# Optimization experiments

Measured on AMD Instinct MI355X. Metric: run time of the kernel, lower is better.

## Reference

```python
import jax, jax.numpy as jnp
import numpy as np

B, N, D, H, L, M, V, F = 4, 2048, 1024, 16, 4, 256, 32000, 4096
DH = D // H  # 64
KEPS = 1e-4  # performer softmax-kernel eps


def layer_norm(x, g, b, eps=1e-5):
    mu = x.mean(-1, keepdims=True)
    var = ((x - mu) ** 2).mean(-1, keepdims=True)
    return (x - mu) * jax.lax.rsqrt(var + eps) * g + b


def softmax_kernel(data, proj, is_query):
    # data: [B,H,N,DH], proj: [M,DH] -> phi(data): [B,H,N,M]
    dn = data.shape[-1] ** -0.25  # d^{-1/4} normalizer
    ratio = proj.shape[0] ** -0.5
    dd = jnp.einsum('bhnd,md->bhnm', dn * data, proj)
    diag = (data * data).sum(-1, keepdims=True) * 0.5 * dn * dn
    if is_query:
        mx = jnp.max(dd, axis=-1, keepdims=True)
    else:
        mx = jnp.max(dd, axis=(-2, -1), keepdims=True)
    return ratio * (jnp.exp(dd - diag - mx) + KEPS)


def setup_inputs() -> dict:
    key = jax.random.key(0)
    ks = iter(jax.random.split(key, 16))
    p = lambda shape: jax.random.normal(next(ks), shape, jnp.float32) * 0.02
    return {
        'x': jax.random.randint(next(ks), (B, N), 0, V, jnp.int32),
        'mask': jnp.ones((B, N), jnp.bool_),
        'tok_emb': p((V, D)),
        'pos_emb': p((N, D)),
        'ln1_g': jnp.ones((L, D), jnp.float32), 'ln1_b': jnp.zeros((L, D), jnp.float32),
        'wq': p((L, D, D)), 'bq': jnp.zeros((L, D), jnp.float32),
        'wk': p((L, D, D)), 'bk': jnp.zeros((L, D), jnp.float32),
        'wv': p((L, D, D)), 'bv': jnp.zeros((L, D), jnp.float32),
        'wo': p((L, D, D)), 'bo': jnp.zeros((L, D), jnp.float32),
        'proj': jax.random.normal(next(ks), (L, M, DH), jnp.float32),
        'ln2_g': jnp.ones((L, D), jnp.float32), 'ln2_b': jnp.zeros((L, D), jnp.float32),
        'w1': p((L, D, F)), 'b1': jnp.zeros((L, F), jnp.float32),
        'w2': p((L, F, D)), 'b2': jnp.zeros((L, D), jnp.float32),
    }


def reference(x, mask, tok_emb, pos_emb, ln1_g, ln1_b, wq, bq, wk, bk, wv, bv,
              wo, bo, proj, ln2_g, ln2_b, w1, b1, w2, b2):
    h = tok_emb[x] + pos_emb[jnp.arange(N)]  # [B,N,D]
    mask4 = mask[:, None, :, None]  # [B,1,N,1]

    def split_heads(t):  # [B,N,D] -> [B,H,N,DH]
        return t.reshape(B, N, H, DH).transpose(0, 2, 1, 3)

    def layer(h, params):
        (g1, c1, Wq, Bq, Wk, Bk, Wv, Bv, Wo, Bo, P, g2, c2, W1, B1, W2, B2) = params
        z = layer_norm(h, g1, c1)
        q = split_heads(z @ Wq + Bq)
        k = split_heads(z @ Wk + Bk)
        v = split_heads(z @ Wv + Bv)
        v = jnp.where(mask4, v, 0.0)  # performer masks only v
        qp = softmax_kernel(q, P, True)   # [B,H,N,M]
        kp = softmax_kernel(k, P, False)  # [B,H,N,M]
        d_inv = 1.0 / jnp.einsum('bhnm,bhm->bhn', qp, kp.sum(-2))
        ctx = jnp.einsum('bhnm,bhnd->bhmd', kp, v)  # [B,H,M,DH]
        attn = jnp.einsum('bhmd,bhnm,bhn->bhnd', ctx, qp, d_inv)
        attn = attn.transpose(0, 2, 1, 3).reshape(B, N, D)
        h = h + attn @ Wo + Bo
        z = layer_norm(h, g2, c2)
        h = h + jax.nn.gelu(z @ W1 + B1, approximate=False) @ W2 + B2
        return h, None

    h, _ = jax.lax.scan(layer, h, (ln1_g, ln1_b, wq, bq, wk, bk, wv, bv,
                                   wo, bo, proj, ln2_g, ln2_b, w1, b1, w2, b2))
    return h.mean(1)  # [B,D]
```

## Files before the change

### kernel.cpp

```cpp
#include <hip/hip_runtime.h>
#include <hip/hip_bf16.h>

typedef unsigned short u16;
typedef unsigned int u32;
typedef __attribute__((ext_vector_type(8))) short short8v;
typedef __attribute__((ext_vector_type(4))) float f32x4;

#define BB    4
#define NN    2048
#define DDIM  1024
#define HH    16
#define DH    64
#define MM    256
#define FDIM  4096
#define LL    4
#define QLD   3072

static constexpr float DN_    = 0.35355339059327373f;
static constexpr float RATIO_ = 0.0625f;
static constexpr float KEPS_  = 1e-4f;

__device__ __forceinline__ short f2bs(float f) {
  __hip_bfloat16 h = __float2bfloat16(f);
  return *(short*)&h;
}
__device__ __forceinline__ float bs2f(short s) {
  return __uint_as_float(((unsigned)(u16)s) << 16);
}
__device__ __forceinline__ float erf_fast(float x) {
  float ax = fabsf(x);
  float t = 1.f / (1.f + 0.3275911f * ax);
  float y = t * (0.254829592f + t * (-0.284496736f + t * (1.421413741f +
            t * (-1.453152027f + t * 1.061405429f))));
  float r = 1.f - y * __expf(-ax * ax);
  return copysignf(r, x);
}

__device__ __forceinline__ void gload_lds16(const void* g, void* l) {
  __builtin_amdgcn_global_load_lds(
      (const __attribute__((address_space(1))) u32*)g,
      (__attribute__((address_space(3))) u32*)l, 16, 0, 0);
}

__global__ __launch_bounds__(256) void k_sentinel(float* __restrict__ out, float val) {
  int i = blockIdx.x * 256 + threadIdx.x;
  if (i < BB * DDIM) out[i] = val;
}

__global__ __launch_bounds__(256) void k_embed_ln(const int* __restrict__ x,
    const float* __restrict__ tok, const float* __restrict__ pos,
    const float* __restrict__ g, const float* __restrict__ b,
    float* __restrict__ h, __hip_bfloat16* __restrict__ zb) {
  int r = blockIdx.x, t = threadIdx.x;
  int n = r & (NN - 1);
  int id = x[r];
  const float* tr = tok + (size_t)id * DDIM;
  const float* pr = pos + (size_t)n * DDIM;
  float* hr = h + (size_t)r * DDIM;
  float v[4], s = 0.f, s2 = 0.f;
#pragma unroll
  for (int i = 0; i < 4; i++) {
    int d = t + i * 256;
    v[i] = tr[d] + pr[d];
    hr[d] = v[i];
    s += v[i]; s2 += v[i] * v[i];
  }
#pragma unroll
  for (int o = 32; o > 0; o >>= 1) { s += __shfl_down(s, o); s2 += __shfl_down(s2, o); }
  __shared__ float ws[8];
  int wid = t >> 6, lane = t & 63;
  if (lane == 0) { ws[wid] = s; ws[4 + wid] = s2; }
  __syncthreads();
  s = ws[0] + ws[1] + ws[2] + ws[3];
  s2 = ws[4] + ws[5] + ws[6] + ws[7];
  float mu = s * (1.f / DDIM);
  float var = s2 * (1.f / DDIM) - mu * mu;
  float rstd = rsqrtf(var + 1e-5f);
  __hip_bfloat16* orow = zb + (size_t)r * DDIM;
#pragma unroll
  for (int i = 0; i < 4; i++) {
    int d = t + i * 256;
    orow[d] = __float2bfloat16((v[i] - mu) * rstd * g[d] + b[d]);
  }
}

__global__ __launch_bounds__(256) void k_ln(const float* __restrict__ in,
    const float* __restrict__ g, const float* __restrict__ b,
    __hip_bfloat16* __restrict__ out) {
  int r = blockIdx.x, t = threadIdx.x;
  const float* xr = in + (size_t)r * DDIM;
  float v[4], s = 0.f, s2 = 0.f;
#pragma unroll
  for (int i = 0; i < 4; i++) {
    v[i] = xr[t + i * 256];
    s += v[i]; s2 += v[i] * v[i];
  }
#pragma unroll
  for (int o = 32; o > 0; o >>= 1) { s += __shfl_down(s, o); s2 += __shfl_down(s2, o); }
  __shared__ float ws[8];
  int wid = t >> 6, lane = t & 63;
  if (lane == 0) { ws[wid] = s; ws[4 + wid] = s2; }
  __syncthreads();
  s = ws[0] + ws[1] + ws[2] + ws[3];
  s2 = ws[4] + ws[5] + ws[6] + ws[7];
  float mu = s * (1.f / DDIM);
  float var = s2 * (1.f / DDIM) - mu * mu;
  float rstd = rsqrtf(var + 1e-5f);
  __hip_bfloat16* orow = out + (size_t)r * DDIM;
#pragma unroll
  for (int i = 0; i < 4; i++) {
    int d = t + i * 256;
    orow[d] = __float2bfloat16((v[i] - mu) * rstd * g[d] + b[d]);
  }
}

__global__ __launch_bounds__(256) void k_wtall(const float* __restrict__ Wq,
    const float* __restrict__ Wk, const float* __restrict__ Wv,
    const float* __restrict__ Wo, const float* __restrict__ W1,
    const float* __restrict__ W2, const float* __restrict__ bq,
    const float* __restrict__ bk, const float* __restrict__ bv,
    __hip_bfloat16* __restrict__ wt, float* __restrict__ bcat) {
  int id = blockIdx.x;
  int t = threadIdx.x;
  if (id >= 3072) {
    int i = (id - 3072) * 256 + t;
    bcat[i] = i < 1024 ? bq[i] : (i < 2048 ? bk[i - 1024] : bv[i - 2048]);
    return;
  }
  const float* W;
  __hip_bfloat16* Wt;
  int K, N, n0, k0;
  if (id < 1024) {
    int which = id >> 8, local = id & 255;
    W = which == 0 ? Wq : which == 1 ? Wk : which == 2 ? Wv : Wo;
    Wt = wt + (size_t)which * 1048576;
    K = 1024; N = 1024;
    n0 = (local & 15) * 64; k0 = (local >> 4) * 64;
  } else if (id < 2048) {
    int local = id - 1024;
    W = W1; Wt = wt + (size_t)4 * 1048576;
    K = 1024; N = 4096;
    n0 = (local & 63) * 64; k0 = (local >> 6) * 64;
  } else {
    int local = id - 2048;
    W = W2; Wt = wt + (size_t)8 * 1048576;
    K = 4096; N = 1024;
    n0 = (local & 15) * 64; k0 = (local >> 4) * 64;
  }
  __shared__ float tl[64][68];
#pragma unroll
  for (int i = 0; i < 4; i++) {
    int kl = (t >> 4) + i * 16;
    float4 f = *(const float4*)&W[(size_t)(k0 + kl) * N + n0 + (t & 15) * 4];
    tl[kl][(t & 15) * 4 + 0] = f.x;
    tl[kl][(t & 15) * 4 + 1] = f.y;
    tl[kl][(t & 15) * 4 + 2] = f.z;
    tl[kl][(t & 15) * 4 + 3] = f.w;
  }
  __syncthreads();
  int nl = t >> 2;
#pragma unroll
  for (int i = 0; i < 4; i++) {
    int kl = (t & 3) * 4 + i * 16;
    size_t ob = (size_t)(n0 + nl) * K + k0 + kl;
    Wt[ob + 0] = __float2bfloat16(tl[kl + 0][nl]);
    Wt[ob + 1] = __float2bfloat16(tl[kl + 1][nl]);
    Wt[ob + 2] = __float2bfloat16(tl[kl + 2][nl]);
    Wt[ob + 3] = __float2bfloat16(tl[kl + 3][nl]);
  }
}

template <bool GELU, bool RES, bool OUTF32>
__global__ __launch_bounds__(256) void k_gemm_mfma(
    const u16* __restrict__ A, const u16* __restrict__ Bt,
    const float* __restrict__ bias, const float* __restrict__ Cin,
    void* __restrict__ Cout, int M, int K, int Nc) {
  __shared__ short As[2][128 * 32];
  __shared__ short Bs[2][128 * 32];
  int t = threadIdx.x;
  int lane = t & 63, w = t >> 6;
  int wr = w >> 1, wc = w & 1;
  int nwg = gridDim.x * gridDim.y;
  int id = blockIdx.y * gridDim.x + blockIdx.x;
  int swz = (id & 7) * (nwg >> 3) + (id >> 3);
  int bx = swz % gridDim.x, by = swz / gridDim.x;
  int row0 = by * 128, col0 = bx * 128;
  f32x4 acc[4][4];
  f32x4 z4 = {0.f, 0.f, 0.f, 0.f};
#pragma unroll
  for (int i = 0; i < 4; i++)
#pragma unroll
    for (int j = 0; j < 4; j++) acc[i][j] = z4;
  int fr = lane & 15;
  int fc = lane >> 4;
  int offA[4], offB[4];
#pragma unroll
  for (int f = 0; f < 4; f++) {
    int ra = wr * 64 + f * 16 + fr;
    offA[f] = ra * 32 + (fc ^ ((ra >> 1) & 3)) * 8;
    int rb = wc * 64 + f * 16 + fr;
    offB[f] = rb * 32 + (fc ^ ((rb >> 1) & 3)) * 8;
  }
  int c0 = t, c1 = 256 + t;
  int r0 = c0 >> 2, cl0 = (c0 & 3) ^ ((r0 >> 1) & 3);
  int r1 = c1 >> 2, cl1 = (c1 & 3) ^ ((r1 >> 1) & 3);
  const u16* pA0 = A + (size_t)(row0 + r0) * K + cl0 * 8;
  const u16* pA1 = A + (size_t)(row0 + r1) * K + cl1 * 8;
  const u16* pB0 = Bt + (size_t)(col0 + r0) * K + cl0 * 8;
  const u16* pB1 = Bt + (size_t)(col0 + r1) * K + cl1 * 8;

  auto STG = [&](short* Ab, short* Bb) {
    gload_lds16(pA0, Ab + c0 * 8);
    gload_lds16(pA1, Ab + c1 * 8);
    gload_lds16(pB0, Bb + c0 * 8);
    gload_lds16(pB1, Bb + c1 * 8);
    pA0 += 32; pA1 += 32; pB0 += 32; pB1 += 32;
  };
  auto COMPUTE = [&](const short* Ab, const short* Bb) {
    short8v af[4], bfr[4];
#pragma unroll
    for (int f = 0; f < 4; f++) {
      af[f] = *(const short8v*)(Ab + offA[f]);
      bfr[f] = *(const short8v*)(Bb + offB[f]);
    }
#pragma unroll
    for (int fi = 0; fi < 4; fi++)
#pragma unroll
      for (int fj = 0; fj < 4; fj++)
        acc[fi][fj] = __builtin_amdgcn_mfma_f32_16x16x32_bf16(
            af[fi], bfr[fj], acc[fi][fj], 0, 0, 0);
  };

  int KT = K >> 5;
  STG(As[0], Bs[0]);
  __syncthreads();
  for (int kt = 0; kt < KT - 2; kt += 2) {
    STG(As[1], Bs[1]);
    COMPUTE(As[0], Bs[0]);
    __syncthreads();
    STG(As[0], Bs[0]);
    COMPUTE(As[1], Bs[1]);
    __syncthreads();
  }
  STG(As[1], Bs[1]);
  COMPUTE(As[0], Bs[0]);
  __syncthreads();
  COMPUTE(As[1], Bs[1]);
#pragma unroll
  for (int fi = 0; fi < 4; fi++) {
#pragma unroll
    for (int fj = 0; fj < 4; fj++) {
#pragma unroll
      for (int ri = 0; ri < 4; ri++) {
        int row = row0 + wr * 64 + fi * 16 + (lane >> 4) * 4 + ri;
        int col = col0 + wc * 64 + fj * 16 + fr;
        float vv = acc[fi][fj][ri] + bias[col];
        if (GELU) vv = 0.5f * vv * (1.f + erf_fast(vv * 0.70710678118f));
        if (RES) vv += Cin[(size_t)row * Nc + col];
        if (OUTF32) ((float*)Cout)[(size_t)row * Nc + col] = vv;
        else ((__hip_bfloat16*)Cout)[(size_t)row * Nc + col] = __float2bfloat16(vv);
      }
    }
  }
}

__global__ __launch_bounds__(256) void k_kv(const u16* __restrict__ kq,
    const u16* __restrict__ vq, const float* __restrict__ P,
    float* __restrict__ es, float* __restrict__ mxc, float* __restrict__ svc,
    float* __restrict__ ctx_part) {
  int bh = blockIdx.x >> 3;
  int chunk = (blockIdx.x >> 1) & 3;
  int mh = blockIdx.x & 1;
  int b = bh >> 4, hh = bh & 15;
  int t = threadIdx.x, lane = t & 63, w = t >> 6;
  int fr = lane & 15, kc = lane >> 4;
  __shared__ short Pl[128 * 64];
  __shared__ short ksl[32 * 64];
  __shared__ short vtl[64 * 32];
  __shared__ short kpl[128 * 32];
  __shared__ float dgs[32];
  __shared__ float wredk[4];
  __shared__ float svl[32][64];
#pragma unroll
  for (int i = 0; i < 4; i++) {
    int e = i * 256 + t;
    int m = e >> 3, j = e & 7;
    const float* src = P + (size_t)(mh * 128 + m) * 64 + j * 8;
    float4 f0 = *(const float4*)src;
    float4 f1 = *(const float4*)(src + 4);
    short* dst = Pl + m * 64 + ((j ^ (m & 7)) << 3);
    dst[0] = f2bs(f0.x); dst[1] = f2bs(f0.y); dst[2] = f2bs(f0.z); dst[3] = f2bs(f0.w);
    dst[4] = f2bs(f1.x); dst[5] = f2bs(f1.y); dst[6] = f2bs(f1.z); dst[7] = f2bs(f1.w);
  }
  f32x4 z4 = {0.f, 0.f, 0.f, 0.f};
  f32x4 accc[2][4];
#pragma unroll
  for (int i = 0; i < 2; i++)
#pragma unroll
    for (int j = 0; j < 4; j++) accc[i][j] = z4;
  float ksp[2] = {0.f, 0.f};
  float svp[8] = {0.f, 0.f, 0.f, 0.f, 0.f, 0.f, 0.f, 0.f};
  float m_run = -3e38f;
  int r8 = t >> 3, j8 = t & 7;
  for (int tile = 0; tile < 16; ++tile) {
    int n0 = chunk * 512 + tile * 32;
    __syncthreads();
    {
      size_t gk = ((size_t)(b * NN) + n0 + r8) * QLD + hh * 64 + j8 * 8;
      short8v k8 = *(const short8v*)(kq + gk);
      *(short8v*)(ksl + r8 * 64 + ((j8 ^ (r8 & 7)) << 3)) = k8;
      float s2 = 0.f;
#pragma unroll
      for (int ii = 0; ii < 8; ii++) { float rv = bs2f(k8[ii]); s2 += rv * rv; }
      s2 += __shfl_down(s2, 4); s2 += __shfl_down(s2, 2); s2 += __shfl_down(s2, 1);
      if (j8 == 0) dgs[r8] = 0.0625f * s2;
      short8v v8 = *(const short8v*)(vq + gk);
#pragma unroll
      for (int ii = 0; ii < 8; ii++) {
        int d = j8 * 8 + ii;
        vtl[d * 32 + (((r8 >> 3) ^ ((d >> 1) & 3)) << 3) + (r8 & 7)] = v8[ii];
        svp[ii] += bs2f(v8[ii]);
      }
    }
    __syncthreads();
    f32x4 accd[2][2];
#pragma unroll
    for (int nt = 0; nt < 2; nt++)
#pragma unroll
      for (int mt = 0; mt < 2; mt++) accd[nt][mt] = z4;
#pragma unroll
    for (int s = 0; s < 2; s++) {
      short8v afr[2];
#pragma unroll
      for (int nt = 0; nt < 2; nt++) {
        int rr = nt * 16 + fr;
        afr[nt] = *(const short8v*)(ksl + rr * 64 + (((s * 4 + kc) ^ (rr & 7)) << 3));
      }
#pragma unroll
      for (int mt = 0; mt < 2; mt++) {
        int ml = w * 32 + mt * 16 + fr;
        short8v bfp = *(const short8v*)(Pl + ml * 64 + (((s * 4 + kc) ^ (ml & 7)) << 3));
#pragma unroll
        for (int nt = 0; nt < 2; nt++)
          accd[nt][mt] = __builtin_amdgcn_mfma_f32_16x16x32_bf16(afr[nt], bfp, accd[nt][mt], 0, 0, 0);
      }
    }
    float tm = -3e38f;
#pragma unroll
    for (int nt = 0; nt < 2; nt++)
#pragma unroll
      for (int mt = 0; mt < 2; mt++) {
        accd[nt][mt] = accd[nt][mt] * DN_;
        tm = fmaxf(tm, fmaxf(fmaxf(accd[nt][mt][0], accd[nt][mt][1]),
                             fmaxf(accd[nt][mt][2], accd[nt][mt][3])));
      }
#pragma unroll
    for (int o = 32; o > 0; o >>= 1) tm = fmaxf(tm, __shfl_xor(tm, o));
    if (lane == 0) wredk[w] = tm;
    __syncthreads();
    float bm = fmaxf(fmaxf(wredk[0], wredk[1]), fmaxf(wredk[2], wredk[3]));
    float nm = fmaxf(m_run, bm);
    float fac = __expf(m_run - nm);
#pragma unroll
    for (int mt = 0; mt < 2; mt++) {
      ksp[mt] *= fac;
#pragma unroll
      for (int dt = 0; dt < 4; dt++) accc[mt][dt] = accc[mt][dt] * fac;
    }
    m_run = nm;
#pragma unroll
    for (int nt = 0; nt < 2; nt++)
#pragma unroll
      for (int mt = 0; mt < 2; mt++)
#pragma unroll
        for (int ri = 0; ri < 4; ri++) {
          int n = nt * 16 + kc * 4 + ri;
          int ml = w * 32 + mt * 16 + fr;
          float kpv = __expf(accd[nt][mt][ri] - dgs[n] - m_run);
          ksp[mt] += kpv;
          kpl[ml * 32 + (((n >> 3) ^ ((ml >> 1) & 3)) << 3) + (n & 7)] = f2bs(kpv);
        }
    short8v bvv[4];
#pragma unroll
    for (int dt = 0; dt < 4; dt++) {
      int d = dt * 16 + fr;
      bvv[dt] = *(const short8v*)(vtl + d * 32 + ((kc ^ ((d >> 1) & 3)) << 3));
    }
#pragma unroll
    for (int mt = 0; mt < 2; mt++) {
      int ml = w * 32 + mt * 16 + fr;
      short8v ak = *(const short8v*)(kpl + ml * 32 + ((kc ^ ((ml >> 1) & 3)) << 3));
#pragma unroll
      for (int dt = 0; dt < 4; dt++)
        accc[mt][dt] = __builtin_amdgcn_mfma_f32_16x16x32_bf16(ak, bvv[dt], accc[mt][dt], 0, 0, 0);
    }
  }
#pragma unroll
  for (int mt = 0; mt < 2; mt++) {
    float vv = ksp[mt];
    vv += __shfl_xor(vv, 16);
    vv += __shfl_xor(vv, 32);
    if (lane < 16)
      es[((size_t)bh * 4 + chunk) * MM + mh * 128 + w * 32 + mt * 16 + lane] = vv;
  }
  if (t == 0) mxc[((size_t)bh * 4 + chunk) * 2 + mh] = m_run;
#pragma unroll
  for (int ii = 0; ii < 8; ii++) svl[r8][j8 * 8 + ii] = svp[ii];
  __syncthreads();
  if (mh == 0 && t < 64) {
    float s = 0.f;
#pragma unroll
    for (int r = 0; r < 32; r++) s += svl[r][t];
    svc[((size_t)bh * 4 + chunk) * 64 + t] = s;
  }
  size_t base = ((size_t)(chunk * 64 + bh)) * MM * DH;
#pragma unroll
  for (int mt = 0; mt < 2; mt++)
#pragma unroll
    for (int dt = 0; dt < 4; dt++)
#pragma unroll
      for (int ri = 0; ri < 4; ri++) {
        int mg = mh * 128 + w * 32 + mt * 16 + kc * 4 + ri;
        int d = dt * 16 + fr;
        ctx_part[base + mg * 64 + d] = accc[mt][dt][ri];
      }
}

__global__ __launch_bounds__(256) void k_ctxred(const float* __restrict__ part,
    const float* __restrict__ es, const float* __restrict__ mxc,
    const float* __restrict__ svc, float* __restrict__ ksum,
    u16* __restrict__ ctxT) {
  int bh = blockIdx.x, t = threadIdx.x;
  __shared__ float tl[64][65];
  __shared__ float facs[8];
  __shared__ float svg[64];
  float mg = -3e38f;
#pragma unroll
  for (int i = 0; i < 8; i++) mg = fmaxf(mg, mxc[(size_t)bh * 8 + i]);
  if (t < 8) facs[t] = __expf(mxc[(size_t)bh * 8 + t] - mg);
  if (t >= 64 && t < 128) {
    int d = t - 64;
    svg[d] = svc[((size_t)bh * 4 + 0) * 64 + d] + svc[((size_t)bh * 4 + 1) * 64 + d] +
             svc[((size_t)bh * 4 + 2) * 64 + d] + svc[((size_t)bh * 4 + 3) * 64 + d];
  }
  __syncthreads();
  {
    size_t eb = (size_t)bh * 4 * MM;
    int mhb = t >> 7;
    float s = es[eb + t] * facs[0 * 2 + mhb] + es[eb + MM + t] * facs[1 * 2 + mhb] +
              es[eb + 2 * MM + t] * facs[2 * 2 + mhb] + es[eb + 3 * MM + t] * facs[3 * 2 + mhb];
    ksum[bh * MM + t] = RATIO_ * (s + KEPS_ * 2048.0f);
  }
  const size_t CH = (size_t)64 * MM * DH;
  for (int mt = 0; mt < 4; mt++) {
    int mhb = mt >> 1;
    float f0 = facs[0 * 2 + mhb], f1 = facs[1 * 2 + mhb];
    float f2 = facs[2 * 2 + mhb], f3 = facs[3 * 2 + mhb];
    __syncthreads();
#pragma unroll
    for (int i = 0; i < 16; i++) {
      int e = i * 256 + t;
      int ml = e >> 6, d = e & 63;
      size_t off = (size_t)bh * MM * DH + (size_t)(mt * 64 + ml) * 64 + d;
      float ev = part[off] * f0 + part[CH + off] * f1 +
                 part[2 * CH + off] * f2 + part[3 * CH + off] * f3;
      tl[ml][d] = RATIO_ * (ev + KEPS_ * svg[d]);
    }
    __syncthreads();
#pragma unroll
    for (int i = 0; i < 16; i++) {
      int e = i * 256 + t;
      int d = e >> 6, ml = e & 63;
      ctxT[((size_t)bh * 64 + d) * 256 + mt * 64 + ml] = (u16)f2bs(tl[ml][d]);
    }
  }
}

__global__ __launch_bounds__(256) void k_attn_fused(const u16* __restrict__ q,
    const float* __restrict__ P, const float* __restrict__ ksum,
    const u16* __restrict__ ctxT, __hip_bfloat16* __restrict__ attn) {
  int bh = blockIdx.x >> 5, rb = blockIdx.x & 31;
  int b = bh >> 4, hh = bh & 15;
  int n0 = rb * 64;
  int t = threadIdx.x, lane = t & 63, w = t >> 6;
  int fr = lane & 15, kc = lane >> 4;
  __shared__ short qsl[64 * 64];
  __shared__ short qpl[64 * 256];
  __shared__ short ctl[64 * 256];
  __shared__ float dgs[64];
  __shared__ float ks_l[MM];
  __shared__ float wred[4][64];
  __shared__ float mx_l[64];
  __shared__ float inv_l[64];
  short8v pf[4][2];
#pragma unroll
  for (int mt = 0; mt < 4; mt++)
#pragma unroll
    for (int s = 0; s < 2; s++) {
      int m = w * 64 + mt * 16 + fr;
      const float* src = P + m * 64 + s * 32 + kc * 8;
      float4 f0 = *(const float4*)src;
      float4 f1 = *(const float4*)(src + 4);
      short8v pv;
      pv[0] = f2bs(f0.x); pv[1] = f2bs(f0.y); pv[2] = f2bs(f0.z); pv[3] = f2bs(f0.w);
      pv[4] = f2bs(f1.x); pv[5] = f2bs(f1.y); pv[6] = f2bs(f1.z); pv[7] = f2bs(f1.w);
      pf[mt][s] = pv;
    }
  ks_l[t] = ksum[bh * MM + t];
  {
    int rr = t >> 2, j4 = t & 3;
    size_t gq = ((size_t)(b * NN) + n0 + rr) * QLD + hh * 64 + j4 * 16;
    short8v q0 = *(const short8v*)(q + gq);
    short8v q1 = *(const short8v*)(q + gq + 8);
    *(short8v*)(qsl + rr * 64 + (((2 * j4) ^ (rr & 7)) << 3)) = q0;
    *(short8v*)(qsl + rr * 64 + (((2 * j4 + 1) ^ (rr & 7)) << 3)) = q1;
    float s2 = 0.f;
#pragma unroll
    for (int ii = 0; ii < 8; ii++) {
      float a = bs2f(q0[ii]), c = bs2f(q1[ii]);
      s2 += a * a + c * c;
    }
    s2 += __shfl_down(s2, 2); s2 += __shfl_down(s2, 1);
    if (j4 == 0) dgs[rr] = 0.0625f * s2;
  }
#pragma unroll
  for (int i = 0; i < 8; i++) {
    int e = i * 256 + t;
    int d = e >> 5, c = e & 31;
    short8v cv = *(const short8v*)(ctxT + ((size_t)bh * 64 + d) * 256 + c * 8);
    *(short8v*)(ctl + d * 256 + ((c ^ (d & 7)) << 3)) = cv;
  }
  __syncthreads();
  f32x4 z4 = {0.f, 0.f, 0.f, 0.f};
  f32x4 accd[4][4];
#pragma unroll
  for (int i = 0; i < 4; i++)
#pragma unroll
    for (int j = 0; j < 4; j++) accd[i][j] = z4;
#pragma unroll
  for (int s = 0; s < 2; s++) {
    short8v afr[4];
#pragma unroll
    for (int nt = 0; nt < 4; nt++) {
      int rr = nt * 16 + fr;
      afr[nt] = *(const short8v*)(qsl + rr * 64 + (((s * 4 + kc) ^ (rr & 7)) << 3));
    }
#pragma unroll
    for (int mt = 0; mt < 4; mt++)
#pragma unroll
      for (int nt = 0; nt < 4; nt++)
        accd[nt][mt] = __builtin_amdgcn_mfma_f32_16x16x32_bf16(afr[nt], pf[mt][s], accd[nt][mt], 0, 0, 0);
  }
#pragma unroll
  for (int i = 0; i < 4; i++)
#pragma unroll
    for (int j = 0; j < 4; j++) accd[i][j] = accd[i][j] * DN_;
  {
    float pmx[16];
#pragma unroll
    for (int nt = 0; nt < 4; nt++)
#pragma unroll
      for (int ri = 0; ri < 4; ri++) {
        float m_ = fmaxf(fmaxf(accd[nt][0][ri], accd[nt][1][ri]),
                         fmaxf(accd[nt][2][ri], accd[nt][3][ri]));
#pragma unroll
        for (int o = 1; o < 16; o <<= 1) m_ = fmaxf(m_, __shfl_xor(m_, o));
        pmx[nt * 4 + ri] = m_;
      }
    if (fr == 0) {
#pragma unroll
      for (int nt = 0; nt < 4; nt++)
#pragma unroll
        for (int ri = 0; ri < 4; ri++)
          wred[w][nt * 16 + kc * 4 + ri] = pmx[nt * 4 + ri];
    }
  }
  __syncthreads();
  if (t < 64)
    mx_l[t] = fmaxf(fmaxf(wred[0][t], wred[1][t]), fmaxf(wred[2][t], wred[3][t]));
  __syncthreads();
  {
    float sp[16];
#pragma unroll
    for (int i = 0; i < 16; i++) sp[i] = 0.f;
#pragma unroll
    for (int nt = 0; nt < 4; nt++)
#pragma unroll
      for (int mt = 0; mt < 4; mt++)
#pragma unroll
        for (int ri = 0; ri < 4; ri++) {
          int n = nt * 16 + kc * 4 + ri;
          int m = w * 64 + mt * 16 + fr;
          float kpv = RATIO_ * (__expf(accd[nt][mt][ri] - dgs[n] - mx_l[n]) + KEPS_);
          sp[nt * 4 + ri] += kpv * ks_l[m];
          int c = m >> 3;
          qpl[n * 256 + ((c ^ (n & 7)) << 3) + (m & 7)] = f2bs(kpv);
        }
#pragma unroll
    for (int i = 0; i < 16; i++) {
#pragma unroll
      for (int o = 1; o < 16; o <<= 1) sp[i] += __shfl_xor(sp[i], o);
    }
    if (fr == 0) {
#pragma unroll
      for (int nt = 0; nt < 4; nt++)
#pragma unroll
        for (int ri = 0; ri < 4; ri++)
          wred[w][nt * 16 + kc * 4 + ri] = sp[nt * 4 + ri];
    }
  }
  __syncthreads();
  if (t < 64)
    inv_l[t] = 1.f / (wred[0][t] + wred[1][t] + wred[2][t] + wred[3][t]);
  __syncthreads();
  f32x4 acc2[4];
#pragma unroll
  for (int dt = 0; dt < 4; dt++) acc2[dt] = z4;
  int nrow = w * 16 + fr;
#pragma unroll
  for (int ks = 0; ks < 8; ks++) {
    int c = ks * 4 + kc;
    short8v aq = *(const short8v*)(qpl + nrow * 256 + ((c ^ (nrow & 7)) << 3));
#pragma unroll
    for (int dt = 0; dt < 4; dt++) {
      int d = dt * 16 + fr;
      short8v bc = *(const short8v*)(ctl + d * 256 + ((c ^ (d & 7)) << 3));
      acc2[dt] = __builtin_amdgcn_mfma_f32_16x16x32_bf16(aq, bc, acc2[dt], 0, 0, 0);
    }
  }
#pragma unroll
  for (int dt = 0; dt < 4; dt++)
#pragma unroll
    for (int ri = 0; ri < 4; ri++) {
      int n = w * 16 + kc * 4 + ri;
      int d = dt * 16 + fr;
      attn[((size_t)(b * NN) + n0 + n) * DDIM + hh * 64 + d] =
          __float2bfloat16(acc2[dt][ri] * inv_l[n]);
    }
}

__global__ __launch_bounds__(256) void k_mean1(const float* __restrict__ h,
                                               float* __restrict__ part) {
  int c = blockIdx.x >> 2, b = blockIdx.x & 3;
  int t = threadIdx.x;
  float s0 = 0.f, s1 = 0.f, s2 = 0.f, s3 = 0.f;
  for (int n = c * 32; n < c * 32 + 32; n++) {
    float4 f = *(const float4*)&h[((size_t)b * NN + n) * DDIM + t * 4];
    s0 += f.x; s1 += f.y; s2 += f.z; s3 += f.w;
  }
  float* p = part + (size_t)c * (BB * DDIM) + b * DDIM + t * 4;
  p[0] = s0; p[1] = s1; p[2] = s2; p[3] = s3;
}
__global__ __launch_bounds__(256) void k_mean2(const float* __restrict__ part,
                                               float* __restrict__ out) {
  int idx = blockIdx.x * 256 + threadIdx.x;
  float s = 0.f;
  for (int c = 0; c < 64; c++) s += part[(size_t)c * (BB * DDIM) + idx];
  out[idx] = s * (1.f / NN);
}

extern "C" void kernel_launch(void* const* d_in, const int* in_sizes, int n_in,
                              void* d_out, int out_size, void* d_ws, size_t ws_size,
                              hipStream_t stream) {
  static const long long EXP[21] = {
      8192, 8192, 32768000, 2097152, 4096, 4096,
      4194304, 4096, 4194304, 4096, 4194304, 4096, 4194304, 4096,
      65536, 4096, 4096, 16777216, 16384, 16777216, 4096
  };
  const size_t NEED_WS = 197559552;
  float sentinel = 0.f;
  if (n_in != 21) {
    sentinel = 100000.f + 100.f * (float)n_in;
  } else {
    for (int i = 0; i < 21; i++)
      if ((long long)in_sizes[i] != EXP[i]) { sentinel = 1000.f + 100.f * i; break; }
  }
  if (sentinel == 0.f && out_size != BB * DDIM) sentinel = 6000.f;
  if (sentinel == 0.f && ws_size < NEED_WS) {
    float units = (float)(ws_size / (32ull << 20));
    if (units > 40.f) units = 40.f;
    sentinel = 5000.f + 100.f * units;
  }
  if (sentinel != 0.f) {
    k_sentinel<<<16, 256, 0, stream>>>((float*)d_out, sentinel);
    return;
  }

  const int* x = (const int*)d_in[0];
  const float* tok  = (const float*)d_in[2];
  const float* pos  = (const float*)d_in[3];
  const float* ln1g = (const float*)d_in[4];
  const float* ln1b = (const float*)d_in[5];
  const float* wq   = (const float*)d_in[6];
  const float* bq   = (const float*)d_in[7];
  const float* wk   = (const float*)d_in[8];
  const float* bk   = (const float*)d_in[9];
  const float* wv   = (const float*)d_in[10];
  const float* bv   = (const float*)d_in[11];
  const float* wo   = (const float*)d_in[12];
  const float* bo   = (const float*)d_in[13];
  const float* proj = (const float*)d_in[14];
  const float* ln2g = (const float*)d_in[15];
  const float* ln2b = (const float*)d_in[16];
  const float* w1   = (const float*)d_in[17];
  const float* b1   = (const float*)d_in[18];
  const float* w2   = (const float*)d_in[19];
  const float* b2   = (const float*)d_in[20];

  const int BN = BB * NN;
  const size_t SZ = (size_t)BN * DDIM;
  const size_t MEG = 1048576;
  float* ws    = (float*)d_ws;
  float* h     = ws;
  u16* qkvb    = (u16*)(ws + SZ);
  __hip_bfloat16* zb   = (__hip_bfloat16*)(ws + 4 * SZ);
  float* ctx   = ws + 4 * SZ + SZ / 2;
  float* ksum  = ctx + (size_t)BB * HH * MM * DH;
  float* bmaxp = ksum + BB * HH * MM;
  float* bcat  = bmaxp + 4096;
  float* mxp   = bmaxp + BB * HH * 128;
  __hip_bfloat16* wt = (__hip_bfloat16*)(mxp + 64);
  float* ctxp  = (float*)(wt + 12 * MEG);
  float* esb   = ctxp + 4 * MEG;
  float* mxcb  = esb + 65536;
  float* svcb  = mxcb + 512;
  u16* ctxT    = (u16*)ctx;
  __hip_bfloat16* ff1b = (__hip_bfloat16*)qkvb;
  __hip_bfloat16* zab  = (__hip_bfloat16*)ctxp;
  float* meanp = ctxp;

  k_embed_ln<<<BN, 256, 0, stream>>>(x, tok, pos, ln1g, ln1b, h, zb);

  for (int l = 0; l < LL; l++) {
    const float* Wq = wq + (size_t)l * DDIM * DDIM;
    const float* Wk = wk + (size_t)l * DDIM * DDIM;
    const float* Wv = wv + (size_t)l * DDIM * DDIM;
    const float* Wo = wo + (size_t)l * DDIM * DDIM;
    const float* W1 = w1 + (size_t)l * DDIM * FDIM;
    const float* W2 = w2 + (size_t)l * FDIM * DDIM;
    const float* Pl = proj + (size_t)l * MM * DH;
    __hip_bfloat16* wtq = wt;
    __hip_bfloat16* wto = wt + 3 * MEG;
    __hip_bfloat16* wt1 = wt + 4 * MEG;
    __hip_bfloat16* wt2 = wt + 8 * MEG;

    k_wtall<<<3084, 256, 0, stream>>>(Wq, Wk, Wv, Wo, W1, W2,
                                      bq + l * DDIM, bk + l * DDIM, bv + l * DDIM,
                                      wt, bcat);

    if (l > 0)
      k_ln<<<BN, 256, 0, stream>>>(h, ln1g + l * DDIM, ln1b + l * DDIM, zb);

    dim3 gQKV(QLD / 128, BN / 128);
    k_gemm_mfma<false, false, false><<<gQKV, 256, 0, stream>>>(
        (const u16*)zb, (const u16*)wtq, bcat, nullptr, qkvb, BN, DDIM, QLD);

    k_kv<<<BB * HH * 8, 256, 0, stream>>>(qkvb + 1024, qkvb + 2048, Pl,
                                          esb, mxcb, svcb, ctxp);
    k_ctxred<<<BB * HH, 256, 0, stream>>>(ctxp, esb, mxcb, svcb, ksum, ctxT);
    k_attn_fused<<<BB * HH * 32, 256, 0, stream>>>(qkvb, Pl, ksum, ctxT, zab);

    dim3 gO(DDIM / 128, BN / 128);
    k_gemm_mfma<false, true, true><<<gO, 256, 0, stream>>>(
        (const u16*)zab, (const u16*)wto, bo + l * DDIM, h, h, BN, DDIM, DDIM);

    k_ln<<<BN, 256, 0, stream>>>(h, ln2g + l * DDIM, ln2b + l * DDIM, zb);
    dim3 g1(FDIM / 128, BN / 128);
    k_gemm_mfma<true, false, false><<<g1, 256, 0, stream>>>(
        (const u16*)zb, (const u16*)wt1, b1 + l * FDIM, nullptr, ff1b, BN, DDIM, FDIM);
    dim3 g2(DDIM / 128, BN / 128);
    k_gemm_mfma<false, true, true><<<g2, 256, 0, stream>>>(
        (const u16*)ff1b, (const u16*)wt2, b2 + l * DDIM, h, h, BN, FDIM, DDIM);
  }

  k_mean1<<<256, 256, 0, stream>>>(h, meanp);
  k_mean2<<<16, 256, 0, stream>>>(meanp, (float*)d_out);
}
```

Measured before the change: 1.822 ms.

## Triple-buffer GEMM LDS staging with partial vmcnt waits

```diff
diff --git a/kernel.cpp b/kernel.cpp
--- a/kernel.cpp
+++ b/kernel.cpp
@@ -41,6 +41,11 @@
       (const __attribute__((address_space(1))) u32*)g,
       (__attribute__((address_space(3))) u32*)l, 16, 0, 0);
 }
+
+#define VMCNT4() asm volatile("s_waitcnt vmcnt(4)" ::: "memory")
+#define VMCNT0() asm volatile("s_waitcnt vmcnt(0)" ::: "memory")
+#define BAR() do { asm volatile("" ::: "memory"); __builtin_amdgcn_s_barrier(); \
+                   asm volatile("" ::: "memory"); } while (0)
 
 __global__ __launch_bounds__(256) void k_sentinel(float* __restrict__ out, float val) {
   int i = blockIdx.x * 256 + threadIdx.x;
@@ -175,8 +180,8 @@
     const u16* __restrict__ A, const u16* __restrict__ Bt,
     const float* __restrict__ bias, const float* __restrict__ Cin,
     void* __restrict__ Cout, int M, int K, int Nc) {
-  __shared__ short As[2][128 * 32];
-  __shared__ short Bs[2][128 * 32];
+  __shared__ short As[3][128 * 32];
+  __shared__ short Bs[3][128 * 32];
   int t = threadIdx.x;
   int lane = t & 63, w = t >> 6;
   int wr = w >> 1, wc = w & 1;
@@ -232,20 +237,21 @@
   };
 
   int KT = K >> 5;
-  STG(As[0], Bs[0]);
-  __syncthreads();
-  for (int kt = 0; kt < KT - 2; kt += 2) {
-    STG(As[1], Bs[1]);
-    COMPUTE(As[0], Bs[0]);
-    __syncthreads();
-    STG(As[0], Bs[0]);
-    COMPUTE(As[1], Bs[1]);
-    __syncthreads();
-  }
-  STG(As[1], Bs[1]);
-  COMPUTE(As[0], Bs[0]);
-  __syncthreads();
-  COMPUTE(As[1], Bs[1]);
+  short *A0 = As[0], *A1 = As[1], *A2 = As[2];
+  short *B0 = Bs[0], *B1 = Bs[1], *B2 = Bs[2];
+  STG(A0, B0);
+  STG(A1, B1);
+  VMCNT4(); BAR();
+  for (int kt = 0; kt < KT - 2; ++kt) {
+    STG(A2, B2);
+    COMPUTE(A0, B0);
+    VMCNT4(); BAR();
+    short* ta = A0; A0 = A1; A1 = A2; A2 = ta;
+    short* tb = B0; B0 = B1; B1 = B2; B2 = tb;
+  }
+  COMPUTE(A0, B0);
+  VMCNT0(); BAR();
+  COMPUTE(A1, B1);
 #pragma unroll
   for (int fi = 0; fi < 4; fi++) {
 #pragma unroll
```

Result: no change. 1.806 ms (-0.9%).

## Pre-swizzle weights into MFMA fragment layout and load B directly to registers

Applied to the files above, without the earlier changes.

```diff
diff --git a/kernel.cpp b/kernel.cpp
--- a/kernel.cpp
+++ b/kernel.cpp
@@ -158,25 +158,28 @@
     tl[kl][(t & 15) * 4 + 3] = f.w;
   }
   __syncthreads();
-  int nl = t >> 2;
-#pragma unroll
-  for (int i = 0; i < 4; i++) {
-    int kl = (t & 3) * 4 + i * 16;
-    size_t ob = (size_t)(n0 + nl) * K + k0 + kl;
-    Wt[ob + 0] = __float2bfloat16(tl[kl + 0][nl]);
-    Wt[ob + 1] = __float2bfloat16(tl[kl + 1][nl]);
-    Wt[ob + 2] = __float2bfloat16(tl[kl + 2][nl]);
-    Wt[ob + 3] = __float2bfloat16(tl[kl + 3][nl]);
+  int g0 = n0 >> 4, kt0 = k0 >> 5, KT = K >> 5;
+  u16* WtU = (u16*)Wt;
+#pragma unroll
+  for (int i = 0; i < 2; i++) {
+    int c = i * 256 + t;
+    int gl = c >> 7;
+    int ktl = (c >> 6) & 1;
+    int l = c & 63;
+    short8v v;
+#pragma unroll
+    for (int j = 0; j < 8; j++)
+      v[j] = f2bs(tl[ktl * 32 + ((l >> 4) << 3) + j][gl * 16 + (l & 15)]);
+    *(short8v*)(WtU + (((size_t)(g0 + gl) * KT + kt0 + ktl) * 512 + l * 8)) = v;
   }
 }
 
 template <bool GELU, bool RES, bool OUTF32>
 __global__ __launch_bounds__(256) void k_gemm_mfma(
-    const u16* __restrict__ A, const u16* __restrict__ Bt,
+    const u16* __restrict__ A, const u16* __restrict__ BtF,
     const float* __restrict__ bias, const float* __restrict__ Cin,
     void* __restrict__ Cout, int M, int K, int Nc) {
   __shared__ short As[2][128 * 32];
-  __shared__ short Bs[2][128 * 32];
   int t = threadIdx.x;
   int lane = t & 63, w = t >> 6;
   int wr = w >> 1, wc = w & 1;
@@ -193,36 +196,39 @@
     for (int j = 0; j < 4; j++) acc[i][j] = z4;
   int fr = lane & 15;
   int fc = lane >> 4;
-  int offA[4], offB[4];
+  int offA[4];
 #pragma unroll
   for (int f = 0; f < 4; f++) {
     int ra = wr * 64 + f * 16 + fr;
     offA[f] = ra * 32 + (fc ^ ((ra >> 1) & 3)) * 8;
-    int rb = wc * 64 + f * 16 + fr;
-    offB[f] = rb * 32 + (fc ^ ((rb >> 1) & 3)) * 8;
   }
   int c0 = t, c1 = 256 + t;
   int r0 = c0 >> 2, cl0 = (c0 & 3) ^ ((r0 >> 1) & 3);
   int r1 = c1 >> 2, cl1 = (c1 & 3) ^ ((r1 >> 1) & 3);
   const u16* pA0 = A + (size_t)(row0 + r0) * K + cl0 * 8;
   const u16* pA1 = A + (size_t)(row0 + r1) * K + cl1 * 8;
-  const u16* pB0 = Bt + (size_t)(col0 + r0) * K + cl0 * 8;
-  const u16* pB1 = Bt + (size_t)(col0 + r1) * K + cl1 * 8;
-
-  auto STG = [&](short* Ab, short* Bb) {
+  int KT = K >> 5;
+  const u16* pB0 = BtF + (size_t)((col0 >> 4) + wc * 4 + 0) * KT * 512 + lane * 8;
+  const u16* pB1 = BtF + (size_t)((col0 >> 4) + wc * 4 + 1) * KT * 512 + lane * 8;
+  const u16* pB2 = BtF + (size_t)((col0 >> 4) + wc * 4 + 2) * KT * 512 + lane * 8;
+  const u16* pB3 = BtF + (size_t)((col0 >> 4) + wc * 4 + 3) * KT * 512 + lane * 8;
+
+  auto STG = [&](short* Ab) {
     gload_lds16(pA0, Ab + c0 * 8);
     gload_lds16(pA1, Ab + c1 * 8);
-    gload_lds16(pB0, Bb + c0 * 8);
-    gload_lds16(pB1, Bb + c1 * 8);
-    pA0 += 32; pA1 += 32; pB0 += 32; pB1 += 32;
+    pA0 += 32; pA1 += 32;
   };
-  auto COMPUTE = [&](const short* Ab, const short* Bb) {
-    short8v af[4], bfr[4];
-#pragma unroll
-    for (int f = 0; f < 4; f++) {
+  auto LDB = [&](short8v (&b)[4]) {
+    b[0] = *(const short8v*)pB0; pB0 += 512;
+    b[1] = *(const short8v*)pB1; pB1 += 512;
+    b[2] = *(const short8v*)pB2; pB2 += 512;
+    b[3] = *(const short8v*)pB3; pB3 += 512;
+  };
+  auto COMPUTE = [&](const short* Ab, const short8v (&bfr)[4]) {
+    short8v af[4];
+#pragma unroll
+    for (int f = 0; f < 4; f++)
       af[f] = *(const short8v*)(Ab + offA[f]);
-      bfr[f] = *(const short8v*)(Bb + offB[f]);
-    }
 #pragma unroll
     for (int fi = 0; fi < 4; fi++)
 #pragma unroll
@@ -231,21 +237,25 @@
             af[fi], bfr[fj], acc[fi][fj], 0, 0, 0);
   };
 
-  int KT = K >> 5;
-  STG(As[0], Bs[0]);
+  short8v b0[4], b1[4];
+  LDB(b0);
+  STG(As[0]);
   __syncthreads();
   for (int kt = 0; kt < KT - 2; kt += 2) {
-    STG(As[1], Bs[1]);
-    COMPUTE(As[0], Bs[0]);
+    LDB(b1);
+    STG(As[1]);
+    COMPUTE(As[0], b0);
     __syncthreads();
-    STG(As[0], Bs[0]);
-    COMPUTE(As[1], Bs[1]);
+    LDB(b0);
+    STG(As[0]);
+    COMPUTE(As[1], b1);
     __syncthreads();
   }
-  STG(As[1], Bs[1]);
-  COMPUTE(As[0], Bs[0]);
-  __syncthreads();
-  COMPUTE(As[1], Bs[1]);
+  LDB(b1);
+  STG(As[1]);
+  COMPUTE(As[0], b0);
+  __syncthreads();
+  COMPUTE(As[1], b1);
 #pragma unroll
   for (int fi = 0; fi < 4; fi++) {
 #pragma unroll
```

After: 1.766 ms. -3.1%, faster.
